# Performance work log

Hardware: AMD Instinct MI355X
Metric: run time of the kernel (lower is better)

The kernel has to match this reference:

```python
import jax, jax.numpy as jnp
import numpy as np

# GLIF3 / AlphaPSC constants from the module __init__
V_TH = -45.0      # v_threshold
V_RESET = -60.0   # v_reset (also used as leak reversal E_L)
C_M = 2.0         # membrane capacitance
TAU = 20.0        # membrane time constant
TAU_REF = 2.0     # refractory period (ms)
K = np.array([0.1, 0.2], dtype=np.float32)          # after-spike-current decay rates
ASC_AMPS = np.array([1.0, -2.0], dtype=np.float32)  # after-spike-current jump amplitudes
TAU_SYN = 5.0     # alpha synapse time constant
DT = 1.0

T, B, NI, NH, NO = 1000, 32, 512, 1024, 256


def setup_inputs() -> dict:
    key = jax.random.key(0)
    k1, k2, k3, k4 = jax.random.split(key, 4)
    x = jax.random.normal(k1, (T, B, NI), dtype=jnp.float32)
    # fc_in scaled up so injected current actually drives spiking from v_reset to v_threshold
    W_in = jax.random.normal(k2, (NH, NI), dtype=jnp.float32) * (50.0 / np.sqrt(NI))
    W_rec = jax.random.normal(k3, (NH, NH), dtype=jnp.float32) * (1.0 / np.sqrt(NH))
    W_out = jax.random.normal(k4, (NO, NH), dtype=jnp.float32) * (1.0 / np.sqrt(NH))
    return {"x": x, "W_in": W_in, "W_rec": W_rec, "W_out": W_out}


def _spike_fn(v):
    # Heaviside forward, sigmoid surrogate gradient (straight-through)
    soft = jax.nn.sigmoid(4.0 * (v - V_TH))
    hard = (v >= V_TH).astype(v.dtype)
    return soft + jax.lax.stop_gradient(hard - soft)


def reference(x, W_in, W_rec, W_out):
    # fc_in: [T,B,NI] @ [NH,NI]^T -> external current per step [T,B,NH]
    I_ext = jnp.einsum('tbi,hi->tbh', x, W_in)

    decay_syn = jnp.float32(np.exp(-DT / TAU_SYN))
    asc_decay = jnp.exp(-jnp.asarray(K) * DT)          # (2,)
    asc_amps = jnp.asarray(ASC_AMPS)                   # (2,)

    v0 = jnp.full((B, NH), V_RESET, dtype=jnp.float32)
    asc0 = jnp.zeros((2, B, NH), dtype=jnp.float32)
    ref0 = jnp.zeros((B, NH), dtype=jnp.float32)
    h0 = jnp.zeros((B, NH), dtype=jnp.float32)
    psc0 = jnp.zeros((B, NH), dtype=jnp.float32)

    def step(carry, I_t):
        v, asc, ref, h, psc = carry
        I = I_t + psc                                   # external + recurrent synaptic current
        asc = asc * asc_decay[:, None, None]            # after-spike currents decay
        # GLIF membrane update: C dv/dt = -C/tau (v - E_L) + I + sum(asc)
        v = v + DT * ((V_RESET - v) / TAU + (I + asc.sum(0)) / C_M)
        in_ref = ref > 0.0
        v = jnp.where(in_ref, V_RESET, v)               # clamp during refractory
        spike = _spike_fn(v) * (1.0 - in_ref.astype(v.dtype))
        v = v * (1.0 - spike) + V_RESET * spike         # hard reset on spike
        asc = asc + spike[None] * asc_amps[:, None, None]
        ref = jnp.where(spike > 0.5, TAU_REF, jnp.maximum(ref - DT, 0.0))
        # DenseConn recurrent projection of spikes, then AlphaPSC two-state filter
        rec = spike @ W_rec.T
        h = decay_syn * h + rec
        psc = decay_syn * psc + DT * h
        return (v, asc, ref, h, psc), spike

    _, spikes = jax.lax.scan(step, (v0, asc0, ref0, h0, psc0), I_ext)  # spikes: [T,B,NH]
    rate = spikes.mean(axis=0)                          # [B,NH]
    return rate @ W_out.T                               # [B,NO]
```

## Files before the change

kernel.cpp:

```cpp
#include <hip/hip_runtime.h>
#include <stdint.h>

#define T_STEPS 1000
#define B_SZ    32
#define NI      512
#define NH      1024
#define NO      256

#define NSLICE  8
#define NBLK    (B_SZ * NSLICE)

typedef unsigned long long u64;

#define OFF_IEXT 0ull
#define SZ_IEXT  ((unsigned long long)T_STEPS * B_SZ * NH * 4ull)
#define OFF_WTS  (OFF_IEXT + SZ_IEXT)
#define SZ_WTS   ((unsigned long long)NH * NH * 4ull)
#define OFF_RATE (OFF_WTS + SZ_WTS)
#define SZ_RATE  ((unsigned long long)B_SZ * NH * 4ull)
#define OFF_SYNC (OFF_RATE + SZ_RATE)
#define SZ_SYNC  ((unsigned long long)2 * B_SZ * NSLICE * 4 * 8ull)

__device__ __forceinline__ u64 ld64_agent(const u64* p) {
  return __hip_atomic_load(p, __ATOMIC_RELAXED, __HIP_MEMORY_SCOPE_AGENT);
}
__device__ __forceinline__ void st64_agent(u64* p, u64 v) {
  __hip_atomic_store(p, v, __ATOMIC_RELAXED, __HIP_MEMORY_SCOPE_AGENT);
}

__global__ __launch_bounds__(256) void prep_wts(const float* __restrict__ Wrec,
                                                float* __restrict__ WTS) {
  __shared__ float tile[64][65];
  const int tid = threadIdx.x;
  const int j0 = blockIdx.x * 64;
  const int i0 = blockIdx.y * 64;
  const int sl = j0 >> 7;
  const int jjb = j0 & 127;
#pragma unroll
  for (int k = 0; k < 16; ++k) {
    const int idx = k * 256 + tid;
    const int jl = idx >> 6, il = idx & 63;
    tile[jl][il] = Wrec[(size_t)(j0 + jl) * NH + i0 + il];
  }
  __syncthreads();
#pragma unroll
  for (int k = 0; k < 16; ++k) {
    const int idx = k * 256 + tid;
    const int il = idx >> 6, jl = idx & 63;
    WTS[((size_t)(sl * NH + i0 + il)) * 128 + jjb + jl] = tile[jl][il];
  }
}

#define GBM 128
#define GBN 128
#define GBK 16
__global__ __launch_bounds__(256) void gemm_in(const float* __restrict__ X,
                                               const float* __restrict__ Win,
                                               float* __restrict__ I) {
  __shared__ float As[GBK][GBM + 4];
  __shared__ float Bs[GBK][GBN + 4];
  const int tid = threadIdx.x;
  const int m0 = blockIdx.x * GBM;
  const int n0 = blockIdx.y * GBN;
  const int tm = tid >> 4, tn = tid & 15;
  const int lr = tid >> 1, lk = (tid & 1) * 8;
  float acc[8][8] = {};
  for (int k0 = 0; k0 < NI; k0 += GBK) {
    float4 a0 = *(const float4*)&X[(size_t)(m0 + lr) * NI + k0 + lk];
    float4 a1 = *(const float4*)&X[(size_t)(m0 + lr) * NI + k0 + lk + 4];
    float4 b0 = *(const float4*)&Win[(size_t)(n0 + lr) * NI + k0 + lk];
    float4 b1 = *(const float4*)&Win[(size_t)(n0 + lr) * NI + k0 + lk + 4];
    As[lk + 0][lr] = a0.x; As[lk + 1][lr] = a0.y; As[lk + 2][lr] = a0.z; As[lk + 3][lr] = a0.w;
    As[lk + 4][lr] = a1.x; As[lk + 5][lr] = a1.y; As[lk + 6][lr] = a1.z; As[lk + 7][lr] = a1.w;
    Bs[lk + 0][lr] = b0.x; Bs[lk + 1][lr] = b0.y; Bs[lk + 2][lr] = b0.z; Bs[lk + 3][lr] = b0.w;
    Bs[lk + 4][lr] = b1.x; Bs[lk + 5][lr] = b1.y; Bs[lk + 6][lr] = b1.z; Bs[lk + 7][lr] = b1.w;
    __syncthreads();
#pragma unroll
    for (int k = 0; k < GBK; ++k) {
      float av[8], bv[8];
      *(float4*)&av[0] = *(const float4*)&As[k][tm * 8];
      *(float4*)&av[4] = *(const float4*)&As[k][tm * 8 + 4];
      *(float4*)&bv[0] = *(const float4*)&Bs[k][tn * 8];
      *(float4*)&bv[4] = *(const float4*)&Bs[k][tn * 8 + 4];
#pragma unroll
      for (int i2 = 0; i2 < 8; ++i2)
#pragma unroll
        for (int j2 = 0; j2 < 8; ++j2) acc[i2][j2] += av[i2] * bv[j2];
    }
    __syncthreads();
  }
#pragma unroll
  for (int i2 = 0; i2 < 8; ++i2) {
    float4 c0 = {acc[i2][0], acc[i2][1], acc[i2][2], acc[i2][3]};
    float4 c1 = {acc[i2][4], acc[i2][5], acc[i2][6], acc[i2][7]};
    *(float4*)&I[(size_t)(m0 + tm * 8 + i2) * NH + n0 + tn * 8] = c0;
    *(float4*)&I[(size_t)(m0 + tm * 8 + i2) * NH + n0 + tn * 8 + 4] = c1;
  }
}

__global__ __launch_bounds__(256) void scan_rsnn(const float* __restrict__ Iext,
                                                 const float* __restrict__ WTS,
                                                 float* __restrict__ rate,
                                                 u64* sync) {
  __shared__ unsigned short slist[NH];
  __shared__ int scnt[2];
  __shared__ float psumB[128];

  const int bid = blockIdx.x;
  const int b   = bid >> 3;
  const int sl  = bid & 7;
  const int tid = threadIdx.x;
  const int wv  = tid >> 6;
  const int ln  = tid & 63;
  const int jloc = tid & 127;

  const float* wts = WTS + (size_t)sl * NH * 128;

  const float D1 = 0.90483741803595957f;
  const float D2 = 0.81873075307798186f;

  float v = -60.0f, A1 = 0.0f, A2 = 0.0f, rf = 0.0f, h = 0.0f, psc = 0.0f;
  float ip = 0.0f;
  int sc = 0;

  if (tid < 128) ip = Iext[(size_t)b * NH + sl * 128 + tid];

  for (int t = 0; t < T_STEPS; ++t) {
    const int par = t & 1;
    u64* gbase = sync + ((size_t)(par * B_SZ + b)) * (NSLICE * 4);

    if (wv < 2) {
      const float I = ip + psc;
      A1 *= D1; A2 *= D2;
      v = v + ((-60.0f - v) / 20.0f + (I + A1 + A2) / 2.0f);
      const bool inref = rf > 0.0f;
      if (inref) v = -60.0f;
      const bool spike = (!inref) && (v >= -45.0f);
      if (spike) { v = -60.0f; A1 += 1.0f; A2 += -2.0f; rf = 2.0f; sc++; }
      else       { rf = fmaxf(rf - 1.0f, 0.0f); }

      const u64 bal = __ballot(spike);
      if (ln < 2) {
        const int w = wv * 2 + ln;
        const unsigned payload = ln ? (unsigned)(bal >> 32) : (unsigned)bal;
        st64_agent(&gbase[sl * 4 + w], (u64)payload | ((u64)(unsigned)(t + 1) << 32));
      }
      __builtin_amdgcn_sched_barrier(0);
      const int tn2 = (t + 1 < T_STEPS) ? t + 1 : t;
      ip = Iext[((size_t)tn2 * B_SZ + b) * NH + sl * 128 + tid];
    } else if (wv == 2) {
      u64 val = 0;
      const u64* gp = &gbase[ln & 31];
      const unsigned want = (unsigned)(t + 1);
      for (;;) {
        if (ln < 32) val = ld64_agent(gp);
        const bool ok = (ln >= 32) || ((unsigned)(val >> 32) == want);
        if (__all(ok)) break;
      }
      unsigned myw = (ln < 32) ? (unsigned)val : 0u;
      int inc = __popc(myw);
#pragma unroll
      for (int d = 1; d < 32; d <<= 1) {
        int y = __shfl_up(inc, d);
        if (ln >= d) inc += y;
      }
      const int cntA = __shfl(inc, 15);
      const int cnt  = __shfl(inc, 31);
      if (ln == 0) { scnt[0] = cntA; scnt[1] = cnt; }
      if (ln < 32) {
        int off = inc - __popc(myw);
        const int base = ln * 32;
        unsigned m = myw;
        while (m) {
          const int bit = __builtin_ctz(m);
          m &= m - 1;
          slist[off++] = (unsigned short)(base + bit);
        }
      }
    }
    __syncthreads();

    float s = 0.0f;
    {
      const int k0 = (tid < 128) ? 0 : scnt[0];
      const int k1 = (tid < 128) ? scnt[0] : scnt[1];
      int k = k0;
      for (; k + 16 <= k1; k += 16) {
        float wv16[16];
#pragma unroll
        for (int m2 = 0; m2 < 16; ++m2)
          wv16[m2] = wts[(size_t)slist[k + m2] * 128 + jloc];
#pragma unroll
        for (int m2 = 0; m2 < 16; ++m2) s += wv16[m2];
      }
      for (; k < k1; ++k) s += wts[(size_t)slist[k] * 128 + jloc];
    }
    if (tid >= 128) psumB[jloc] = s;
    __syncthreads();

    if (tid < 128) {
      const float rec = s + psumB[tid];
      h = D2 * h + rec;
      psc = D2 * psc + h;
    }
  }

  if (tid < 128) rate[(size_t)b * NH + sl * 128 + tid] = (float)sc / 1000.0f;
}

__global__ __launch_bounds__(256) void out_gemv(const float* __restrict__ rate,
                                                const float* __restrict__ Wout,
                                                float* __restrict__ out) {
  __shared__ float rs[NH];
  const int b = blockIdx.x, tid = threadIdx.x;
  for (int i = tid; i < NH; i += 256) rs[i] = rate[(size_t)b * NH + i];
  __syncthreads();
  const float* wr = Wout + (size_t)tid * NH;
  float s = 0.0f;
  for (int hh = 0; hh < NH; hh += 4) {
    float4 w4 = *(const float4*)&wr[hh];
    s += rs[hh] * w4.x + rs[hh + 1] * w4.y + rs[hh + 2] * w4.z + rs[hh + 3] * w4.w;
  }
  out[(size_t)b * NO + tid] = s;
}

extern "C" void kernel_launch(void* const* d_in, const int* in_sizes, int n_in,
                              void* d_out, int out_size, void* d_ws, size_t ws_size,
                              hipStream_t stream) {
  const float* x    = (const float*)d_in[0];
  const float* Win  = (const float*)d_in[1];
  const float* Wrec = (const float*)d_in[2];
  const float* Wout = (const float*)d_in[3];
  float* out = (float*)d_out;

  char* ws = (char*)d_ws;
  float* Iext = (float*)(ws + OFF_IEXT);
  float* WTS  = (float*)(ws + OFF_WTS);
  float* rate = (float*)(ws + OFF_RATE);
  u64*   sync = (u64*)(ws + OFF_SYNC);

  prep_wts<<<dim3(16, 16), dim3(256), 0, stream>>>(Wrec, WTS);
  gemm_in<<<dim3((T_STEPS * B_SZ) / GBM, NH / GBN), dim3(256), 0, stream>>>(x, Win, Iext);
  scan_rsnn<<<dim3(NBLK), dim3(256), 0, stream>>>(Iext, WTS, rate, sync);
  out_gemv<<<dim3(B_SZ), dim3(256), 0, stream>>>(rate, Wout, out);
}
```

Measured before the change: 3.975 ms.

## Keep recurrent weight slice resident in LDS with 32-neuron by 4-batch blocks

Repartitions the persistent scan kernel so each block owns 32 hidden neurons for 4 batch elements, 256 blocks in total. The block's 1024x32 slice of W_rec (about 132 KB) is loaded once into shared memory, so per-step spike gathers read LDS instead of global/L2 memory, and the separate transpose kernel goes away. Every block now polls 32 flags per batch element, one per neuron group, and builds four spike lists in parallel. The cost is high LDS use, which limits occupancy to one block per CU, plus more cross-block sync traffic per step.

```diff
diff --git a/kernel.cpp b/kernel.cpp
--- a/kernel.cpp
+++ b/kernel.cpp
@@ -7,48 +7,26 @@
 #define NH      1024
 #define NO      256
 
-#define NSLICE  8
-#define NBLK    (B_SZ * NSLICE)
+#define JBLK    32
+#define BBATCH  4
+#define NJG     (NH / JBLK)
+#define NBG     (B_SZ / BBATCH)
+#define NBLK    (NJG * NBG)
 
 typedef unsigned long long u64;
 
 #define OFF_IEXT 0ull
-#define SZ_IEXT  ((unsigned long long)T_STEPS * B_SZ * NH * 4ull)
-#define OFF_WTS  (OFF_IEXT + SZ_IEXT)
-#define SZ_WTS   ((unsigned long long)NH * NH * 4ull)
-#define OFF_RATE (OFF_WTS + SZ_WTS)
-#define SZ_RATE  ((unsigned long long)B_SZ * NH * 4ull)
+#define SZ_IEXT  ((u64)T_STEPS * B_SZ * NH * 4ull)
+#define OFF_RATE (OFF_IEXT + SZ_IEXT)
+#define SZ_RATE  ((u64)B_SZ * NH * 4ull)
 #define OFF_SYNC (OFF_RATE + SZ_RATE)
-#define SZ_SYNC  ((unsigned long long)2 * B_SZ * NSLICE * 4 * 8ull)
+#define SZ_SYNC  ((u64)2 * B_SZ * NJG * 8ull)
 
 __device__ __forceinline__ u64 ld64_agent(const u64* p) {
   return __hip_atomic_load(p, __ATOMIC_RELAXED, __HIP_MEMORY_SCOPE_AGENT);
 }
 __device__ __forceinline__ void st64_agent(u64* p, u64 v) {
   __hip_atomic_store(p, v, __ATOMIC_RELAXED, __HIP_MEMORY_SCOPE_AGENT);
-}
-
-__global__ __launch_bounds__(256) void prep_wts(const float* __restrict__ Wrec,
-                                                float* __restrict__ WTS) {
-  __shared__ float tile[64][65];
-  const int tid = threadIdx.x;
-  const int j0 = blockIdx.x * 64;
-  const int i0 = blockIdx.y * 64;
-  const int sl = j0 >> 7;
-  const int jjb = j0 & 127;
-#pragma unroll
-  for (int k = 0; k < 16; ++k) {
-    const int idx = k * 256 + tid;
-    const int jl = idx >> 6, il = idx & 63;
-    tile[jl][il] = Wrec[(size_t)(j0 + jl) * NH + i0 + il];
-  }
-  __syncthreads();
-#pragma unroll
-  for (int k = 0; k < 16; ++k) {
-    const int idx = k * 256 + tid;
-    const int il = idx >> 6, jl = idx & 63;
-    WTS[((size_t)(sl * NH + i0 + il)) * 128 + jjb + jl] = tile[jl][il];
-  }
 }
 
 #define GBM 128
@@ -99,22 +77,30 @@
 }
 
 __global__ __launch_bounds__(256) void scan_rsnn(const float* __restrict__ Iext,
-                                                 const float* __restrict__ WTS,
+                                                 const float* __restrict__ Wrec,
                                                  float* __restrict__ rate,
                                                  u64* sync) {
-  __shared__ unsigned short slist[NH];
-  __shared__ int scnt[2];
+  __shared__ float WL[NH][JBLK + 1];
+  __shared__ unsigned short slist[BBATCH][NH];
+  __shared__ int scnt[BBATCH][2];
   __shared__ float psumB[128];
 
   const int bid = blockIdx.x;
-  const int b   = bid >> 3;
-  const int sl  = bid & 7;
+  const int jg  = bid & (NJG - 1);
+  const int bg  = bid >> 5;
+  const int j0  = jg * JBLK;
+  const int b0  = bg * BBATCH;
   const int tid = threadIdx.x;
   const int wv  = tid >> 6;
   const int ln  = tid & 63;
-  const int jloc = tid & 127;
-
-  const float* wts = WTS + (size_t)sl * NH * 128;
+  const int bl  = (tid >> 5) & 3;
+  const int jl  = tid & 31;
+
+  for (int k = 0; k < 128; ++k) {
+    const int jj = k >> 2;
+    const int i  = ((k & 3) << 8) | tid;
+    WL[i][jj] = Wrec[(size_t)(j0 + jj) * NH + i];
+  }
 
   const float D1 = 0.90483741803595957f;
   const float D2 = 0.81873075307798186f;
@@ -122,14 +108,14 @@
   float v = -60.0f, A1 = 0.0f, A2 = 0.0f, rf = 0.0f, h = 0.0f, psc = 0.0f;
   float ip = 0.0f;
   int sc = 0;
-
-  if (tid < 128) ip = Iext[(size_t)b * NH + sl * 128 + tid];
+  if (tid < 128) ip = Iext[(size_t)(b0 + bl) * NH + j0 + jl];
+  __syncthreads();
 
   for (int t = 0; t < T_STEPS; ++t) {
     const int par = t & 1;
-    u64* gbase = sync + ((size_t)(par * B_SZ + b)) * (NSLICE * 4);
-
-    if (wv < 2) {
+    u64* sbase = sync + (size_t)par * B_SZ * NJG;
+
+    if (tid < 128) {
       const float I = ip + psc;
       A1 *= D1; A2 *= D2;
       v = v + ((-60.0f - v) / 20.0f + (I + A1 + A2) / 2.0f);
@@ -140,72 +126,72 @@
       else       { rf = fmaxf(rf - 1.0f, 0.0f); }
 
       const u64 bal = __ballot(spike);
-      if (ln < 2) {
-        const int w = wv * 2 + ln;
-        const unsigned payload = ln ? (unsigned)(bal >> 32) : (unsigned)bal;
-        st64_agent(&gbase[sl * 4 + w], (u64)payload | ((u64)(unsigned)(t + 1) << 32));
+      if ((ln & 31) == 0) {
+        const int bb = b0 + wv * 2 + (ln >> 5);
+        const unsigned payload = (ln >= 32) ? (unsigned)(bal >> 32) : (unsigned)bal;
+        st64_agent(&sbase[(size_t)bb * NJG + jg],
+                   (u64)payload | ((u64)(unsigned)(t + 1) << 32));
       }
       __builtin_amdgcn_sched_barrier(0);
+
+      u64 val;
+      {
+        const u64* gp = &sbase[(size_t)(b0 + bl) * NJG + jl];
+        const unsigned want = (unsigned)(t + 1);
+        do { val = ld64_agent(gp); } while ((unsigned)(val >> 32) != want);
+      }
+      unsigned myw = (unsigned)val;
+
+      int inc = __popc(myw);
+#pragma unroll
+      for (int d = 1; d < 32; d <<= 1) {
+        const int y = __shfl_up(inc, d);
+        if ((ln & 31) >= d) inc += y;
+      }
+      if ((ln & 31) == 15) scnt[bl][0] = inc;
+      if ((ln & 31) == 31) scnt[bl][1] = inc;
+      int off = inc - __popc(myw);
+      const int base = jl * 32;
+      while (myw) {
+        const int bit = __builtin_ctz(myw);
+        myw &= myw - 1;
+        slist[bl][off++] = (unsigned short)(base + bit);
+      }
+    }
+    __syncthreads();
+
+    float ipn = ip;
+    if (tid < 128) {
       const int tn2 = (t + 1 < T_STEPS) ? t + 1 : t;
-      ip = Iext[((size_t)tn2 * B_SZ + b) * NH + sl * 128 + tid];
-    } else if (wv == 2) {
-      u64 val = 0;
-      const u64* gp = &gbase[ln & 31];
-      const unsigned want = (unsigned)(t + 1);
-      for (;;) {
-        if (ln < 32) val = ld64_agent(gp);
-        const bool ok = (ln >= 32) || ((unsigned)(val >> 32) == want);
-        if (__all(ok)) break;
-      }
-      unsigned myw = (ln < 32) ? (unsigned)val : 0u;
-      int inc = __popc(myw);
-#pragma unroll
-      for (int d = 1; d < 32; d <<= 1) {
-        int y = __shfl_up(inc, d);
-        if (ln >= d) inc += y;
-      }
-      const int cntA = __shfl(inc, 15);
-      const int cnt  = __shfl(inc, 31);
-      if (ln == 0) { scnt[0] = cntA; scnt[1] = cnt; }
-      if (ln < 32) {
-        int off = inc - __popc(myw);
-        const int base = ln * 32;
-        unsigned m = myw;
-        while (m) {
-          const int bit = __builtin_ctz(m);
-          m &= m - 1;
-          slist[off++] = (unsigned short)(base + bit);
-        }
-      }
-    }
-    __syncthreads();
+      ipn = Iext[((size_t)tn2 * B_SZ + b0 + bl) * NH + j0 + jl];
+    }
 
     float s = 0.0f;
     {
-      const int k0 = (tid < 128) ? 0 : scnt[0];
-      const int k1 = (tid < 128) ? scnt[0] : scnt[1];
+      const int k0 = (tid < 128) ? 0 : scnt[bl][0];
+      const int k1 = (tid < 128) ? scnt[bl][0] : scnt[bl][1];
       int k = k0;
-      for (; k + 16 <= k1; k += 16) {
-        float wv16[16];
-#pragma unroll
-        for (int m2 = 0; m2 < 16; ++m2)
-          wv16[m2] = wts[(size_t)slist[k + m2] * 128 + jloc];
-#pragma unroll
-        for (int m2 = 0; m2 < 16; ++m2) s += wv16[m2];
-      }
-      for (; k < k1; ++k) s += wts[(size_t)slist[k] * 128 + jloc];
-    }
-    if (tid >= 128) psumB[jloc] = s;
+      for (; k + 8 <= k1; k += 8) {
+        float w8[8];
+#pragma unroll
+        for (int m = 0; m < 8; ++m) w8[m] = WL[slist[bl][k + m]][jl];
+#pragma unroll
+        for (int m = 0; m < 8; ++m) s += w8[m];
+      }
+      for (; k < k1; ++k) s += WL[slist[bl][k]][jl];
+    }
+    if (tid >= 128) psumB[tid - 128] = s;
     __syncthreads();
 
     if (tid < 128) {
       const float rec = s + psumB[tid];
       h = D2 * h + rec;
       psc = D2 * psc + h;
-    }
-  }
-
-  if (tid < 128) rate[(size_t)b * NH + sl * 128 + tid] = (float)sc / 1000.0f;
+      ip = ipn;
+    }
+  }
+
+  if (tid < 128) rate[(size_t)(b0 + bl) * NH + j0 + jl] = (float)sc / 1000.0f;
 }
 
 __global__ __launch_bounds__(256) void out_gemv(const float* __restrict__ rate,
@@ -235,12 +221,10 @@
 
   char* ws = (char*)d_ws;
   float* Iext = (float*)(ws + OFF_IEXT);
-  float* WTS  = (float*)(ws + OFF_WTS);
   float* rate = (float*)(ws + OFF_RATE);
   u64*   sync = (u64*)(ws + OFF_SYNC);
 
-  prep_wts<<<dim3(16, 16), dim3(256), 0, stream>>>(Wrec, WTS);
   gemm_in<<<dim3((T_STEPS * B_SZ) / GBM, NH / GBN), dim3(256), 0, stream>>>(x, Win, Iext);
-  scan_rsnn<<<dim3(NBLK), dim3(256), 0, stream>>>(Iext, WTS, rate, sync);
+  scan_rsnn<<<dim3(NBLK), dim3(256), 0, stream>>>(Iext, Wrec, rate, sync);
   out_gemv<<<dim3(B_SZ), dim3(256), 0, stream>>>(rate, Wout, out);
 }
```

New measurement: 4.570 ms. 1.15x slower.
